# Optimization experiments

Hardware: AMD Instinct MI355X
Metric: run time of the kernel (lower is better)

The kernel has to match this reference:

```python
import jax, jax.numpy as jnp
import numpy as np

N, MA, F, NF = 512, 64, 128, 16
UPDATE_RATIO = 0.1
DECAY = 1.0
EPS = 1e-12  # avoids NaN grad of sqrt at self-distance 0 (torch diagonal is masked out by exp anyway)


def setup_inputs() -> dict:
    key = jax.random.key(0)
    ks = jax.random.split(key, 8)
    z = jax.random.randint(ks[0], (N, MA), 0, 10, dtype=jnp.int64) if jax.config.jax_enable_x64 else jax.random.randint(ks[0], (N, MA), 0, 10, dtype=jnp.int32)
    # pad last few atoms of each molecule with -1 to exercise the mask
    z = z.at[:, MA - 8:].set(-1)
    r = jax.random.normal(ks[1], (N, MA, 3), dtype=jnp.float32) * 3.0
    h = jax.random.normal(ks[2], (N, MA, F), dtype=jnp.float32)
    distances = jnp.linspace(0.5, 6.0, NF, dtype=jnp.float32)
    widths = jax.random.uniform(ks[3], (NF,), dtype=jnp.float32) * 0.5 + 0.5  # keep sigma > 0
    din = F * (1 + NF)  # 2176
    W1 = jax.random.normal(ks[4], (din, 512), dtype=jnp.float32) * (1.0 / np.sqrt(din))
    b1 = jnp.zeros((512,), dtype=jnp.float32)
    W2 = jax.random.normal(ks[5], (512, F), dtype=jnp.float32) * (1.0 / np.sqrt(512.0))
    b2 = jnp.zeros((F,), dtype=jnp.float32)
    return {"z": z, "r": r, "h": h, "distances": distances, "widths": widths,
            "W1": W1, "b1": b1, "W2": W2, "b2": b2}


def reference(z, r, h, distances, widths, W1, b1, W2, b2):
    n, ma = z.shape
    nf = distances.shape[0]
    # pairwise distance: (n, ma, ma)
    dv = r[:, :, None, :] - r[:, None, :, :]
    d = jnp.sqrt(jnp.sum(dv * dv, axis=-1) + EPS)
    mu = distances.reshape(1, nf, 1, 1)
    sigma = widths.reshape(1, nf, 1, 1)
    mask1 = (z > -1).astype(h.dtype)                      # (n, ma)
    pair_mask = mask1[:, :, None] * mask1[:, None, :]     # (n, ma, ma)
    # Gaussian RBF scores, masked: (n, nf, ma, ma)
    w = pair_mask[:, None] * jnp.exp(-((d[:, None] - mu) ** 2) / sigma) * 5.0
    # aggregate neighbor features: (n, ma, nf, F) -> (n, ma, nf*F)
    u = jnp.einsum('nfab,nbc->nafc', w, h).reshape(n, ma, nf * h.shape[-1])
    v = jnp.concatenate([h, u], axis=2)                   # (n, ma, F*(1+nf))
    v = jax.nn.silu(v @ W1 + b1) @ W2 + b2                # MLP 'net'
    h_new = h + v * UPDATE_RATIO * DECAY * mask1[:, :, None]
    return (z, r, h_new)
```

## Files before the change

### kernel.cpp

```cpp
#include <hip/hip_runtime.h>

#define MA 64
#define F 128
#define NF 16
#define HID 512
#define LDUB 144
#define LDWB 144
#define LDT1B 1040
#define UB0 0
#define UB1 9216
#define WL0 18432
#define WL1 27648

typedef float  float4v __attribute__((ext_vector_type(4)));
typedef short  short8  __attribute__((ext_vector_type(8)));
typedef int    int8v   __attribute__((ext_vector_type(8)));

static __device__ __forceinline__ unsigned int pack2bf(float x, float y) {
    unsigned int a = __float_as_uint(x) + 0x8000u;
    unsigned int b = __float_as_uint(y) + 0x8000u;
    return __builtin_amdgcn_perm(b, a, 0x07060302u);
}
static __device__ __forceinline__ unsigned short f2bf1(float x) {
    return (unsigned short)((__float_as_uint(x) + 0x8000u) >> 16);
}
static __device__ __forceinline__ unsigned int pk4fp8(float a, float b, float c, float d) {
    int p = __builtin_amdgcn_cvt_pk_fp8_f32(a, b, 0, false);
    p = __builtin_amdgcn_cvt_pk_fp8_f32(c, d, p, true);
    return (unsigned int)p;
}

#define LGKM_BAR() do {                                        \
    asm volatile("s_waitcnt lgkmcnt(0)" ::: "memory");         \
    __builtin_amdgcn_s_barrier();                              \
    asm volatile("" ::: "memory");                             \
} while (0)

__global__ void pack_frags(const float* __restrict__ W1, const float* __restrict__ W2,
                           unsigned char* __restrict__ w1p, unsigned short* __restrict__ w2p) {
    int gid  = blockIdx.x * 4 + (threadIdx.x >> 6);
    int lane = threadIdx.x & 63;
    int arow = lane & 15;
    int kq   = lane >> 4;
    if (gid < 544) {
        int kt = gid >> 5, jt = gid & 31;
        const float* base = W1 + (size_t)(kt * 128 + kq * 32) * HID + jt * 16 + arow;
        unsigned int o[8];
        #pragma unroll
        for (int p = 0; p < 8; p++)
            o[p] = pk4fp8(base[(p * 4 + 0) * HID], base[(p * 4 + 1) * HID],
                          base[(p * 4 + 2) * HID], base[(p * 4 + 3) * HID]);
        unsigned char* dst = w1p + ((size_t)gid * 64 + lane) * 32;
        *(uint4*)dst        = (uint4){o[0], o[1], o[2], o[3]};
        *(uint4*)(dst + 16) = (uint4){o[4], o[5], o[6], o[7]};
    } else if (gid < 544 + 128) {
        int g2 = gid - 544;
        int kt = g2 >> 3, mt = g2 & 7;
        const float* base = W2 + (size_t)(kt * 32 + kq * 8) * F + mt * 16 + arow;
        short8 o;
        #pragma unroll
        for (int j = 0; j < 8; j++) o[j] = (short)f2bf1(base[j * F]);
        *(short8*)(w2p + ((size_t)g2 * 64 + lane) * 8) = o;
    }
}

__launch_bounds__(1024, 4)
__global__ void node_conv_mfma(const int* __restrict__ z, const float* __restrict__ rr,
        const float* __restrict__ h, const float* __restrict__ dist,
        const float* __restrict__ wid, const float* __restrict__ b1,
        const float* __restrict__ b2,
        const unsigned char* __restrict__ w1p, const unsigned short* __restrict__ w2p,
        float* __restrict__ out) {
    const int n = blockIdx.x;
    const int tid = threadIdx.x;
    const int lane = tid & 63;
    const int wave = tid >> 6;
    const int arow = lane & 15;
    const int quad = lane >> 4;
    const int kgrp = quad * 8;
    const int whi = wave >> 1;
    const int wlo = wave & 1;

    __shared__ __attribute__((aligned(16))) unsigned char lds[66560];
    __shared__ float r_lds[MA][5];

    const int N = gridDim.x;
    const float* hg = h + (size_t)n * MA * F;

    if (tid < MA) {
        int zi = z[n * MA + tid];
        out[(size_t)n * MA + tid] = (float)zi;
        r_lds[tid][0] = rr[(n * MA + tid) * 3 + 0];
        r_lds[tid][1] = rr[(n * MA + tid) * 3 + 1];
        r_lds[tid][2] = rr[(n * MA + tid) * 3 + 2];
        r_lds[tid][3] = (zi > -1) ? 1.0f : 0.0f;
    }
    if (tid < MA * 3)
        out[(size_t)N * MA + (size_t)n * MA * 3 + tid] = rr[(size_t)n * MA * 3 + tid];

    for (int i = tid; i < MA * F / 4; i += 1024) {
        float4 v = ((const float4*)hg)[i];
        int a = i >> 5, c4 = (i & 31) * 4;
        *(unsigned int*)&lds[UB0 + a * LDUB + c4] = pk4fp8(v.x, v.y, v.z, v.w);
    }
    short8 ah[2];
    {
        int c = whi * 16 + arow;
        #pragma unroll
        for (int ks2 = 0; ks2 < 2; ks2++)
            #pragma unroll
            for (int j = 0; j < 8; j++)
                ah[ks2][j] = (short)f2bf1(hg[(size_t)(ks2 * 32 + kgrp + j) * F + c]);
    }
    __syncthreads();

    const int wa = tid >> 4;
    const int wb0 = (tid & 15) * 4;
    float dpre[4];
    {
        float ax = r_lds[wa][0], ay = r_lds[wa][1], az = r_lds[wa][2];
        float am = r_lds[wa][3];
        #pragma unroll
        for (int j = 0; j < 4; j++) {
            float dx = ax - r_lds[wb0 + j][0];
            float dy = ay - r_lds[wb0 + j][1];
            float dz = az - r_lds[wb0 + j][2];
            float d = sqrtf(dx * dx + dy * dy + dz * dz + 1e-12f);
            float mm = am * r_lds[wb0 + j][3];
            dpre[j] = d + (1.0f - mm) * 1e4f;
        }
    }

    {
        float mu = dist[0];
        float isg = 1.0f / wid[0];
        float e[4];
        #pragma unroll
        for (int j = 0; j < 4; j++) {
            float t = dpre[j] - mu;
            e[j] = 5.0f * __expf(-t * t * isg);
        }
        uint2 wp = { pack2bf(e[0], e[1]), pack2bf(e[2], e[3]) };
        *(uint2*)&lds[WL0 + wa * LDWB + wb0 * 2] = wp;
    }
    int8v afr[2];
    {
        const unsigned char* p0 = w1p + ((size_t)((wave * 2) * 64 + lane)) * 32;
        afr[0] = *(const int8v*)p0;
        afr[1] = *(const int8v*)(p0 + 2048);
    }
    LGKM_BAR();

    const float4v zf = {0.f, 0.f, 0.f, 0.f};
    float4v acc[2][4];
    #pragma unroll
    for (int i = 0; i < 2; i++)
        #pragma unroll
        for (int jv = 0; jv < 4; jv++) acc[i][jv] = zf;

    for (int f = 0; f <= NF; f++) {
        const int sel = f & 1;
        const int ubR = sel ? UB1 : UB0;
        const int ubW = sel ? UB0 : UB1;
        const int wlR = sel ? WL1 : WL0;
        const int wlW = sel ? WL0 : WL1;

        #pragma unroll
        for (int at = 0; at < 4; at++) {
            int8v bfr = *(const int8v*)&lds[ubR + (at * 16 + arow) * LDUB + quad * 32];
            acc[0][at] = __builtin_amdgcn_mfma_scale_f32_16x16x128_f8f6f4(
                afr[0], bfr, acc[0][at], 0, 0, 0, 127, 0, 127);
            acc[1][at] = __builtin_amdgcn_mfma_scale_f32_16x16x128_f8f6f4(
                afr[1], bfr, acc[1][at], 0, 0, 0, 127, 0, 127);
        }

        if (f < NF) {
            const unsigned char* pN = w1p + ((size_t)(((f + 1) * 32 + wave * 2) * 64 + lane)) * 32;
            afr[0] = *(const int8v*)pN;
            afr[1] = *(const int8v*)(pN + 2048);

            float4v ud0 = zf, ud1 = zf;
            #pragma unroll
            for (int ks2 = 0; ks2 < 2; ks2++) {
                short8 bw0 = *(const short8*)&lds[wlR + ((wlo * 2 + 0) * 16 + arow) * LDWB + (ks2 * 32 + kgrp) * 2];
                ud0 = __builtin_amdgcn_mfma_f32_16x16x32_bf16(ah[ks2], bw0, ud0, 0, 0, 0);
                short8 bw1 = *(const short8*)&lds[wlR + ((wlo * 2 + 1) * 16 + arow) * LDWB + (ks2 * 32 + kgrp) * 2];
                ud1 = __builtin_amdgcn_mfma_f32_16x16x32_bf16(ah[ks2], bw1, ud1, 0, 0, 0);
            }
            unsigned int u0 = pk4fp8(ud0[0], ud0[1], ud0[2], ud0[3]);
            unsigned int u1 = pk4fp8(ud1[0], ud1[1], ud1[2], ud1[3]);
            *(unsigned int*)&lds[ubW + ((wlo * 2 + 0) * 16 + arow) * LDUB + whi * 16 + quad * 4] = u0;
            *(unsigned int*)&lds[ubW + ((wlo * 2 + 1) * 16 + arow) * LDUB + whi * 16 + quad * 4] = u1;

            if (f <= NF - 2) {
                float mu = dist[f + 1];
                float isg = 1.0f / wid[f + 1];
                float e[4];
                #pragma unroll
                for (int j = 0; j < 4; j++) {
                    float t = dpre[j] - mu;
                    e[j] = 5.0f * __expf(-t * t * isg);
                }
                uint2 wp = { pack2bf(e[0], e[1]), pack2bf(e[2], e[3]) };
                *(uint2*)&lds[wlW + wa * LDWB + wb0 * 2] = wp;
            }
        }
        LGKM_BAR();
    }

    float4 b1v[2];
    #pragma unroll
    for (int mt = 0; mt < 2; mt++)
        b1v[mt] = *(const float4*)&b1[wave * 32 + mt * 16 + quad * 4];

    #pragma unroll
    for (int mt = 0; mt < 2; mt++) {
        #pragma unroll
        for (int at = 0; at < 4; at++) {
            float xs[4];
            #pragma unroll
            for (int r = 0; r < 4; r++) {
                float x = acc[mt][at][r] + ((const float*)&b1v[mt])[r];
                xs[r] = x / (1.0f + __expf(-x));
            }
            uint2 pv = { pack2bf(xs[0], xs[1]), pack2bf(xs[2], xs[3]) };
            *(uint2*)&lds[(at * 16 + arow) * LDT1B + (wave * 32 + mt * 16 + quad * 4) * 2] = pv;
        }
    }
    LGKM_BAR();

    float4v g2[2] = { zf, zf };

    short8 awA = *(const short8*)(w2p + ((size_t)(whi) * 64 + lane) * 8);
    #pragma unroll
    for (int ks2 = 0; ks2 < 8; ks2++) {
        const int k1 = 2 * ks2 + 1;
        short8 awB = *(const short8*)(w2p + ((size_t)(k1 * 8 + whi) * 64 + lane) * 8);
        #pragma unroll
        for (int j = 0; j < 2; j++) {
            short8 bt = *(const short8*)&lds[((wlo * 2 + j) * 16 + arow) * LDT1B + ((2 * ks2) * 32 + kgrp) * 2];
            g2[j] = __builtin_amdgcn_mfma_f32_16x16x32_bf16(awA, bt, g2[j], 0, 0, 0);
        }
        const int k2 = (ks2 < 7) ? 2 * ks2 + 2 : 0;
        awA = *(const short8*)(w2p + ((size_t)(k2 * 8 + whi) * 64 + lane) * 8);
        #pragma unroll
        for (int j = 0; j < 2; j++) {
            short8 bt = *(const short8*)&lds[((wlo * 2 + j) * 16 + arow) * LDT1B + ((2 * ks2 + 1) * 32 + kgrp) * 2];
            g2[j] = __builtin_amdgcn_mfma_f32_16x16x32_bf16(awB, bt, g2[j], 0, 0, 0);
        }
    }

    float* outh = out + (size_t)N * MA * 4 + (size_t)n * MA * F;
    const int c0 = whi * 16 + quad * 4;
    float4 b2v = *(const float4*)&b2[c0];
    #pragma unroll
    for (int j = 0; j < 2; j++) {
        int a = (wlo * 2 + j) * 16 + arow;
        float m = r_lds[a][3] * 0.1f;
        float4 hv = *(const float4*)&hg[a * F + c0];
        float4 res;
        res.x = hv.x + (g2[j][0] + b2v.x) * m;
        res.y = hv.y + (g2[j][1] + b2v.y) * m;
        res.z = hv.z + (g2[j][2] + b2v.z) * m;
        res.w = hv.w + (g2[j][3] + b2v.w) * m;
        *(float4*)&outh[(size_t)a * F + c0] = res;
    }
}

extern "C" void kernel_launch(void* const* d_in, const int* in_sizes, int n_in,
                              void* d_out, int out_size, void* d_ws, size_t ws_size,
                              hipStream_t stream) {
    const int*   z    = (const int*)d_in[0];
    const float* rr   = (const float*)d_in[1];
    const float* h    = (const float*)d_in[2];
    const float* dist = (const float*)d_in[3];
    const float* wid  = (const float*)d_in[4];
    const float* W1   = (const float*)d_in[5];
    const float* b1   = (const float*)d_in[6];
    const float* W2   = (const float*)d_in[7];
    const float* b2   = (const float*)d_in[8];
    float* out = (float*)d_out;

    int Nmol = in_sizes[0] / MA;

    unsigned char*  w1p = (unsigned char*)d_ws;
    unsigned short* w2p = (unsigned short*)(w1p + (size_t)544 * 64 * 32);

    pack_frags<<<168, 256, 0, stream>>>(W1, W2, w1p, w2p);
    node_conv_mfma<<<Nmol, 1024, 0, stream>>>(z, rr, h, dist, wid, b1, b2, w1p, w2p, out);
}
```

Before: 144.6 us.

## Split block into producer and consumer waves for RBF aggregation and W1 GEMM

Warp-specializes the 16-wave block. Waves 0-7 act as consumers that run the fp8 W1 MFMA accumulation with four 16-row hidden tiles each. Waves 8-15 act as producers that compute the RBF weights and the per-filter neighbour aggregation u into the double-buffered LDS tiles. Previously every wave did both jobs in each filter iteration; the split is meant to overlap the aggregation with the main GEMM. In exchange each consumer holds twice the accumulators and each producer holds four h fragments, which raises register pressure, and half of the waves now sit idle in each phase.

```diff
diff --git a/kernel.cpp b/kernel.cpp
--- a/kernel.cpp
+++ b/kernel.cpp
@@ -80,6 +80,7 @@
     const int kgrp = quad * 8;
     const int whi = wave >> 1;
     const int wlo = wave & 1;
+    const bool consumer = wave < 8;
 
     __shared__ __attribute__((aligned(16))) unsigned char lds[66560];
     __shared__ float r_lds[MA][5];
@@ -103,130 +104,158 @@
         int a = i >> 5, c4 = (i & 31) * 4;
         *(unsigned int*)&lds[UB0 + a * LDUB + c4] = pk4fp8(v.x, v.y, v.z, v.w);
     }
-    short8 ah[2];
-    {
-        int c = whi * 16 + arow;
-        #pragma unroll
-        for (int ks2 = 0; ks2 < 2; ks2++)
-            #pragma unroll
-            for (int j = 0; j < 8; j++)
-                ah[ks2][j] = (short)f2bf1(hg[(size_t)(ks2 * 32 + kgrp + j) * F + c]);
-    }
-    __syncthreads();
-
-    const int wa = tid >> 4;
-    const int wb0 = (tid & 15) * 4;
-    float dpre[4];
-    {
-        float ax = r_lds[wa][0], ay = r_lds[wa][1], az = r_lds[wa][2];
-        float am = r_lds[wa][3];
-        #pragma unroll
-        for (int j = 0; j < 4; j++) {
-            float dx = ax - r_lds[wb0 + j][0];
-            float dy = ay - r_lds[wb0 + j][1];
-            float dz = az - r_lds[wb0 + j][2];
-            float d = sqrtf(dx * dx + dy * dy + dz * dz + 1e-12f);
-            float mm = am * r_lds[wb0 + j][3];
-            dpre[j] = d + (1.0f - mm) * 1e4f;
-        }
-    }
-
-    {
-        float mu = dist[0];
-        float isg = 1.0f / wid[0];
-        float e[4];
-        #pragma unroll
-        for (int j = 0; j < 4; j++) {
-            float t = dpre[j] - mu;
-            e[j] = 5.0f * __expf(-t * t * isg);
-        }
-        uint2 wp = { pack2bf(e[0], e[1]), pack2bf(e[2], e[3]) };
-        *(uint2*)&lds[WL0 + wa * LDWB + wb0 * 2] = wp;
-    }
-    int8v afr[2];
-    {
-        const unsigned char* p0 = w1p + ((size_t)((wave * 2) * 64 + lane)) * 32;
-        afr[0] = *(const int8v*)p0;
-        afr[1] = *(const int8v*)(p0 + 2048);
-    }
-    LGKM_BAR();
 
     const float4v zf = {0.f, 0.f, 0.f, 0.f};
-    float4v acc[2][4];
-    #pragma unroll
-    for (int i = 0; i < 2; i++)
-        #pragma unroll
-        for (int jv = 0; jv < 4; jv++) acc[i][jv] = zf;
-
-    for (int f = 0; f <= NF; f++) {
-        const int sel = f & 1;
-        const int ubR = sel ? UB1 : UB0;
-        const int ubW = sel ? UB0 : UB1;
-        const int wlR = sel ? WL1 : WL0;
-        const int wlW = sel ? WL0 : WL1;
-
-        #pragma unroll
-        for (int at = 0; at < 4; at++) {
-            int8v bfr = *(const int8v*)&lds[ubR + (at * 16 + arow) * LDUB + quad * 32];
-            acc[0][at] = __builtin_amdgcn_mfma_scale_f32_16x16x128_f8f6f4(
-                afr[0], bfr, acc[0][at], 0, 0, 0, 127, 0, 127);
-            acc[1][at] = __builtin_amdgcn_mfma_scale_f32_16x16x128_f8f6f4(
-                afr[1], bfr, acc[1][at], 0, 0, 0, 127, 0, 127);
-        }
-
-        if (f < NF) {
-            const unsigned char* pN = w1p + ((size_t)(((f + 1) * 32 + wave * 2) * 64 + lane)) * 32;
-            afr[0] = *(const int8v*)pN;
-            afr[1] = *(const int8v*)(pN + 2048);
-
-            float4v ud0 = zf, ud1 = zf;
-            #pragma unroll
-            for (int ks2 = 0; ks2 < 2; ks2++) {
-                short8 bw0 = *(const short8*)&lds[wlR + ((wlo * 2 + 0) * 16 + arow) * LDWB + (ks2 * 32 + kgrp) * 2];
-                ud0 = __builtin_amdgcn_mfma_f32_16x16x32_bf16(ah[ks2], bw0, ud0, 0, 0, 0);
-                short8 bw1 = *(const short8*)&lds[wlR + ((wlo * 2 + 1) * 16 + arow) * LDWB + (ks2 * 32 + kgrp) * 2];
-                ud1 = __builtin_amdgcn_mfma_f32_16x16x32_bf16(ah[ks2], bw1, ud1, 0, 0, 0);
-            }
-            unsigned int u0 = pk4fp8(ud0[0], ud0[1], ud0[2], ud0[3]);
-            unsigned int u1 = pk4fp8(ud1[0], ud1[1], ud1[2], ud1[3]);
-            *(unsigned int*)&lds[ubW + ((wlo * 2 + 0) * 16 + arow) * LDUB + whi * 16 + quad * 4] = u0;
-            *(unsigned int*)&lds[ubW + ((wlo * 2 + 1) * 16 + arow) * LDUB + whi * 16 + quad * 4] = u1;
-
-            if (f <= NF - 2) {
-                float mu = dist[f + 1];
-                float isg = 1.0f / wid[f + 1];
-                float e[4];
+
+    if (consumer) {
+        const int ci = wave;
+        const int jbase = ci * 4;
+
+        int8v p0, p1, p2, p3;
+        {
+            const unsigned char* pp = w1p + ((size_t)(jbase * 64 + lane)) * 32;
+            p0 = *(const int8v*)pp;
+            p1 = *(const int8v*)(pp + 2048);
+        }
+        __syncthreads();
+        LGKM_BAR();
+
+        float4v acc[4][4];
+        #pragma unroll
+        for (int i = 0; i < 4; i++)
+            #pragma unroll
+            for (int jv = 0; jv < 4; jv++) acc[i][jv] = zf;
+
+        for (int f = 0; f <= NF; f++) {
+            const int ubR = (f & 1) ? UB1 : UB0;
+            const unsigned char* pseg = w1p + ((size_t)((f * 32 + jbase) * 64 + lane)) * 32;
+
+            p2 = *(const int8v*)(pseg + 2 * 2048);
+            p3 = *(const int8v*)(pseg + 3 * 2048);
+
+            #pragma unroll
+            for (int at = 0; at < 4; at++) {
+                int8v bfr = *(const int8v*)&lds[ubR + (at * 16 + arow) * LDUB + quad * 32];
+                acc[0][at] = __builtin_amdgcn_mfma_scale_f32_16x16x128_f8f6f4(
+                    p0, bfr, acc[0][at], 0, 0, 0, 127, 0, 127);
+                acc[1][at] = __builtin_amdgcn_mfma_scale_f32_16x16x128_f8f6f4(
+                    p1, bfr, acc[1][at], 0, 0, 0, 127, 0, 127);
+            }
+            #pragma unroll
+            for (int at = 0; at < 4; at++) {
+                int8v bfr = *(const int8v*)&lds[ubR + (at * 16 + arow) * LDUB + quad * 32];
+                acc[2][at] = __builtin_amdgcn_mfma_scale_f32_16x16x128_f8f6f4(
+                    p2, bfr, acc[2][at], 0, 0, 0, 127, 0, 127);
+                acc[3][at] = __builtin_amdgcn_mfma_scale_f32_16x16x128_f8f6f4(
+                    p3, bfr, acc[3][at], 0, 0, 0, 127, 0, 127);
+            }
+            if (f < NF) {
+                const unsigned char* pN = w1p + ((size_t)(((f + 1) * 32 + jbase) * 64 + lane)) * 32;
+                p0 = *(const int8v*)pN;
+                p1 = *(const int8v*)(pN + 2048);
+            }
+            LGKM_BAR();
+        }
+
+        #pragma unroll
+        for (int jj = 0; jj < 4; jj++) {
+            float4 b1v = *(const float4*)&b1[(jbase + jj) * 16 + quad * 4];
+            #pragma unroll
+            for (int at = 0; at < 4; at++) {
+                float xs[4];
                 #pragma unroll
-                for (int j = 0; j < 4; j++) {
-                    float t = dpre[j] - mu;
-                    e[j] = 5.0f * __expf(-t * t * isg);
+                for (int r = 0; r < 4; r++) {
+                    float x = acc[jj][at][r] + ((const float*)&b1v)[r];
+                    xs[r] = x / (1.0f + __expf(-x));
                 }
-                uint2 wp = { pack2bf(e[0], e[1]), pack2bf(e[2], e[3]) };
-                *(uint2*)&lds[wlW + wa * LDWB + wb0 * 2] = wp;
-            }
+                uint2 pv = { pack2bf(xs[0], xs[1]), pack2bf(xs[2], xs[3]) };
+                *(uint2*)&lds[(at * 16 + arow) * LDT1B + ((jbase + jj) * 16 + quad * 4) * 2] = pv;
+            }
+        }
+    } else {
+        const int pi = wave - 8;
+        const int uat = pi & 3;
+        const int uc0 = (pi >> 2) * 4;
+        const int pt  = tid - 512;
+        const int wa  = pt >> 3;
+        const int wb0 = (pt & 7) * 8;
+
+        short8 ah2[4][2];
+        #pragma unroll
+        for (int cc = 0; cc < 4; cc++) {
+            int c = (uc0 + cc) * 16 + arow;
+            #pragma unroll
+            for (int ks2 = 0; ks2 < 2; ks2++)
+                #pragma unroll
+                for (int j = 0; j < 8; j++)
+                    ah2[cc][ks2][j] = (short)f2bf1(hg[(size_t)(ks2 * 32 + kgrp + j) * F + c]);
+        }
+        __syncthreads();
+
+        float dpre[8];
+        {
+            float ax = r_lds[wa][0], ay = r_lds[wa][1], az = r_lds[wa][2];
+            float am = r_lds[wa][3];
+            #pragma unroll
+            for (int j = 0; j < 8; j++) {
+                float dx = ax - r_lds[wb0 + j][0];
+                float dy = ay - r_lds[wb0 + j][1];
+                float dz = az - r_lds[wb0 + j][2];
+                float d = sqrtf(dx * dx + dy * dy + dz * dz + 1e-12f);
+                float mm = am * r_lds[wb0 + j][3];
+                dpre[j] = d + (1.0f - mm) * 1e4f;
+            }
+        }
+        {
+            float mu = dist[0];
+            float isg = 1.0f / wid[0];
+            float e[8];
+            #pragma unroll
+            for (int j = 0; j < 8; j++) {
+                float t = dpre[j] - mu;
+                e[j] = 5.0f * __expf(-t * t * isg);
+            }
+            uint4 wp = { pack2bf(e[0], e[1]), pack2bf(e[2], e[3]),
+                         pack2bf(e[4], e[5]), pack2bf(e[6], e[7]) };
+            *(uint4*)&lds[WL0 + wa * LDWB + wb0 * 2] = wp;
         }
         LGKM_BAR();
-    }
-
-    float4 b1v[2];
-    #pragma unroll
-    for (int mt = 0; mt < 2; mt++)
-        b1v[mt] = *(const float4*)&b1[wave * 32 + mt * 16 + quad * 4];
-
-    #pragma unroll
-    for (int mt = 0; mt < 2; mt++) {
-        #pragma unroll
-        for (int at = 0; at < 4; at++) {
-            float xs[4];
-            #pragma unroll
-            for (int r = 0; r < 4; r++) {
-                float x = acc[mt][at][r] + ((const float*)&b1v[mt])[r];
-                xs[r] = x / (1.0f + __expf(-x));
-            }
-            uint2 pv = { pack2bf(xs[0], xs[1]), pack2bf(xs[2], xs[3]) };
-            *(uint2*)&lds[(at * 16 + arow) * LDT1B + (wave * 32 + mt * 16 + quad * 4) * 2] = pv;
-        }
-    }
+
+        for (int f = 0; f <= NF; f++) {
+            const int sel = f & 1;
+            const int ubW = sel ? UB0 : UB1;
+            const int wlR = sel ? WL1 : WL0;
+            const int wlW = sel ? WL0 : WL1;
+
+            if (f < NF) {
+                short8 bw0 = *(const short8*)&lds[wlR + (uat * 16 + arow) * LDWB + (0 * 32 + kgrp) * 2];
+                short8 bw1 = *(const short8*)&lds[wlR + (uat * 16 + arow) * LDWB + (1 * 32 + kgrp) * 2];
+                #pragma unroll
+                for (int cc = 0; cc < 4; cc++) {
+                    float4v ud = zf;
+                    ud = __builtin_amdgcn_mfma_f32_16x16x32_bf16(ah2[cc][0], bw0, ud, 0, 0, 0);
+                    ud = __builtin_amdgcn_mfma_f32_16x16x32_bf16(ah2[cc][1], bw1, ud, 0, 0, 0);
+                    unsigned int up = pk4fp8(ud[0], ud[1], ud[2], ud[3]);
+                    *(unsigned int*)&lds[ubW + (uat * 16 + arow) * LDUB + (uc0 + cc) * 16 + quad * 4] = up;
+                }
+                if (f <= NF - 2) {
+                    float mu = dist[f + 1];
+                    float isg = 1.0f / wid[f + 1];
+                    float e[8];
+                    #pragma unroll
+                    for (int j = 0; j < 8; j++) {
+                        float t = dpre[j] - mu;
+                        e[j] = 5.0f * __expf(-t * t * isg);
+                    }
+                    uint4 wp = { pack2bf(e[0], e[1]), pack2bf(e[2], e[3]),
+                                 pack2bf(e[4], e[5]), pack2bf(e[6], e[7]) };
+                    *(uint4*)&lds[wlW + wa * LDWB + wb0 * 2] = wp;
+                }
+            }
+            LGKM_BAR();
+        }
+    }
+
     LGKM_BAR();
 
     float4v g2[2] = { zf, zf };
```

Result: slower. 211.3 us (+46.1%).

## Process two feature chunks per pipeline stage to halve barrier count

Applied to the files above, without the earlier changes.

Restructures the per-filter loop so each iteration consumes two U chunks (two K-slices of the first-layer MFMA) and produces the next two, with doubled LDS buffers. This halves the number of workgroup barriers and adds more independent MFMA work between syncs, and the W1 fragment loads are split into two prefetched register sets. The cost is more LDS (73728 bytes), which may reduce occupancy, and more live registers, with a prologue and epilogue to handle the odd chunk count.

```diff
diff --git a/kernel.cpp b/kernel.cpp
--- a/kernel.cpp
+++ b/kernel.cpp
@@ -7,10 +7,12 @@
 #define LDUB 144
 #define LDWB 144
 #define LDT1B 1040
-#define UB0 0
-#define UB1 9216
-#define WL0 18432
-#define WL1 27648
+#define UBA 0
+#define UBB 18432
+#define WLA 36864
+#define WLB 55296
+#define UBT 9216
+#define WLT 9216
 
 typedef float  float4v __attribute__((ext_vector_type(4)));
 typedef short  short8  __attribute__((ext_vector_type(8)));
@@ -81,7 +83,7 @@
     const int whi = wave >> 1;
     const int wlo = wave & 1;
 
-    __shared__ __attribute__((aligned(16))) unsigned char lds[66560];
+    __shared__ __attribute__((aligned(16))) unsigned char lds[73728];
     __shared__ float r_lds[MA][5];
 
     const int N = gridDim.x;
@@ -101,7 +103,7 @@
     for (int i = tid; i < MA * F / 4; i += 1024) {
         float4 v = ((const float4*)hg)[i];
         int a = i >> 5, c4 = (i & 31) * 4;
-        *(unsigned int*)&lds[UB0 + a * LDUB + c4] = pk4fp8(v.x, v.y, v.z, v.w);
+        *(unsigned int*)&lds[UBA + a * LDUB + c4] = pk4fp8(v.x, v.y, v.z, v.w);
     }
     short8 ah[2];
     {
@@ -111,6 +113,12 @@
             #pragma unroll
             for (int j = 0; j < 8; j++)
                 ah[ks2][j] = (short)f2bf1(hg[(size_t)(ks2 * 32 + kgrp + j) * F + c]);
+    }
+    int8v p0, p1, q0, q1;
+    {
+        const unsigned char* pp = w1p + ((size_t)((wave * 2) * 64 + lane)) * 32;
+        p0 = *(const int8v*)pp;
+        p1 = *(const int8v*)(pp + 2048);
     }
     __syncthreads();
 
@@ -131,9 +139,9 @@
         }
     }
 
-    {
-        float mu = dist[0];
-        float isg = 1.0f / wid[0];
+    auto EXPW = [&](int fidx, int wlOff) {
+        float mu = dist[fidx];
+        float isg = 1.0f / wid[fidx];
         float e[4];
         #pragma unroll
         for (int j = 0; j < 4; j++) {
@@ -141,72 +149,88 @@
             e[j] = 5.0f * __expf(-t * t * isg);
         }
         uint2 wp = { pack2bf(e[0], e[1]), pack2bf(e[2], e[3]) };
-        *(uint2*)&lds[WL0 + wa * LDWB + wb0 * 2] = wp;
-    }
-    int8v afr[2];
-    {
-        const unsigned char* p0 = w1p + ((size_t)((wave * 2) * 64 + lane)) * 32;
-        afr[0] = *(const int8v*)p0;
-        afr[1] = *(const int8v*)(p0 + 2048);
-    }
+        *(uint2*)&lds[wlOff + wa * LDWB + wb0 * 2] = wp;
+    };
+    const float4v zf = {0.f, 0.f, 0.f, 0.f};
+    auto UG = [&](int wlOff, int ubOff) {
+        float4v ud0 = zf, ud1 = zf;
+        #pragma unroll
+        for (int ks2 = 0; ks2 < 2; ks2++) {
+            short8 bw0 = *(const short8*)&lds[wlOff + ((wlo * 2 + 0) * 16 + arow) * LDWB + (ks2 * 32 + kgrp) * 2];
+            ud0 = __builtin_amdgcn_mfma_f32_16x16x32_bf16(ah[ks2], bw0, ud0, 0, 0, 0);
+            short8 bw1 = *(const short8*)&lds[wlOff + ((wlo * 2 + 1) * 16 + arow) * LDWB + (ks2 * 32 + kgrp) * 2];
+            ud1 = __builtin_amdgcn_mfma_f32_16x16x32_bf16(ah[ks2], bw1, ud1, 0, 0, 0);
+        }
+        unsigned int u0 = pk4fp8(ud0[0], ud0[1], ud0[2], ud0[3]);
+        unsigned int u1 = pk4fp8(ud1[0], ud1[1], ud1[2], ud1[3]);
+        *(unsigned int*)&lds[ubOff + ((wlo * 2 + 0) * 16 + arow) * LDUB + whi * 16 + quad * 4] = u0;
+        *(unsigned int*)&lds[ubOff + ((wlo * 2 + 1) * 16 + arow) * LDUB + whi * 16 + quad * 4] = u1;
+    };
+
+    EXPW(0, WLB);
+    EXPW(1, WLA);
+    EXPW(2, WLA + WLT);
     LGKM_BAR();
-
-    const float4v zf = {0.f, 0.f, 0.f, 0.f};
+    UG(WLB, UBA + UBT);
+    LGKM_BAR();
+
     float4v acc[2][4];
     #pragma unroll
     for (int i = 0; i < 2; i++)
         #pragma unroll
         for (int jv = 0; jv < 4; jv++) acc[i][jv] = zf;
 
-    for (int f = 0; f <= NF; f++) {
-        const int sel = f & 1;
-        const int ubR = sel ? UB1 : UB0;
-        const int ubW = sel ? UB0 : UB1;
-        const int wlR = sel ? WL1 : WL0;
-        const int wlW = sel ? WL0 : WL1;
-
+    for (int i = 0; i < 8; i++) {
+        const int sel = i & 1;
+        const int ubR = sel ? UBB : UBA;
+        const int ubW = sel ? UBA : UBB;
+        const int wlR = sel ? WLB : WLA;
+        const int wlW = sel ? WLA : WLB;
+
+        {
+            const unsigned char* pq = w1p + ((size_t)(((2 * i + 1) * 32 + wave * 2) * 64 + lane)) * 32;
+            q0 = *(const int8v*)pq;
+            q1 = *(const int8v*)(pq + 2048);
+        }
         #pragma unroll
         for (int at = 0; at < 4; at++) {
             int8v bfr = *(const int8v*)&lds[ubR + (at * 16 + arow) * LDUB + quad * 32];
             acc[0][at] = __builtin_amdgcn_mfma_scale_f32_16x16x128_f8f6f4(
-                afr[0], bfr, acc[0][at], 0, 0, 0, 127, 0, 127);
+                p0, bfr, acc[0][at], 0, 0, 0, 127, 0, 127);
             acc[1][at] = __builtin_amdgcn_mfma_scale_f32_16x16x128_f8f6f4(
-                afr[1], bfr, acc[1][at], 0, 0, 0, 127, 0, 127);
-        }
-
-        if (f < NF) {
-            const unsigned char* pN = w1p + ((size_t)(((f + 1) * 32 + wave * 2) * 64 + lane)) * 32;
-            afr[0] = *(const int8v*)pN;
-            afr[1] = *(const int8v*)(pN + 2048);
-
-            float4v ud0 = zf, ud1 = zf;
-            #pragma unroll
-            for (int ks2 = 0; ks2 < 2; ks2++) {
-                short8 bw0 = *(const short8*)&lds[wlR + ((wlo * 2 + 0) * 16 + arow) * LDWB + (ks2 * 32 + kgrp) * 2];
-                ud0 = __builtin_amdgcn_mfma_f32_16x16x32_bf16(ah[ks2], bw0, ud0, 0, 0, 0);
-                short8 bw1 = *(const short8*)&lds[wlR + ((wlo * 2 + 1) * 16 + arow) * LDWB + (ks2 * 32 + kgrp) * 2];
-                ud1 = __builtin_amdgcn_mfma_f32_16x16x32_bf16(ah[ks2], bw1, ud1, 0, 0, 0);
-            }
-            unsigned int u0 = pk4fp8(ud0[0], ud0[1], ud0[2], ud0[3]);
-            unsigned int u1 = pk4fp8(ud1[0], ud1[1], ud1[2], ud1[3]);
-            *(unsigned int*)&lds[ubW + ((wlo * 2 + 0) * 16 + arow) * LDUB + whi * 16 + quad * 4] = u0;
-            *(unsigned int*)&lds[ubW + ((wlo * 2 + 1) * 16 + arow) * LDUB + whi * 16 + quad * 4] = u1;
-
-            if (f <= NF - 2) {
-                float mu = dist[f + 1];
-                float isg = 1.0f / wid[f + 1];
-                float e[4];
-                #pragma unroll
-                for (int j = 0; j < 4; j++) {
-                    float t = dpre[j] - mu;
-                    e[j] = 5.0f * __expf(-t * t * isg);
-                }
-                uint2 wp = { pack2bf(e[0], e[1]), pack2bf(e[2], e[3]) };
-                *(uint2*)&lds[wlW + wa * LDWB + wb0 * 2] = wp;
-            }
-        }
+                p1, bfr, acc[1][at], 0, 0, 0, 127, 0, 127);
+        }
+        #pragma unroll
+        for (int at = 0; at < 4; at++) {
+            int8v bfr = *(const int8v*)&lds[ubR + UBT + (at * 16 + arow) * LDUB + quad * 32];
+            acc[0][at] = __builtin_amdgcn_mfma_scale_f32_16x16x128_f8f6f4(
+                q0, bfr, acc[0][at], 0, 0, 0, 127, 0, 127);
+            acc[1][at] = __builtin_amdgcn_mfma_scale_f32_16x16x128_f8f6f4(
+                q1, bfr, acc[1][at], 0, 0, 0, 127, 0, 127);
+        }
+        {
+            const unsigned char* pp = w1p + ((size_t)(((2 * i + 2) * 32 + wave * 2) * 64 + lane)) * 32;
+            p0 = *(const int8v*)pp;
+            p1 = *(const int8v*)(pp + 2048);
+        }
+
+        UG(wlR, ubW);
+        if (2 * i + 2 <= NF - 1) UG(wlR + WLT, ubW + UBT);
+        if (2 * i + 3 <= NF - 1) EXPW(2 * i + 3, wlW);
+        if (2 * i + 4 <= NF - 1) EXPW(2 * i + 4, wlW + WLT);
+
         LGKM_BAR();
     }
+
+    #pragma unroll
+    for (int at = 0; at < 4; at++) {
+        int8v bfr = *(const int8v*)&lds[UBA + (at * 16 + arow) * LDUB + quad * 32];
+        acc[0][at] = __builtin_amdgcn_mfma_scale_f32_16x16x128_f8f6f4(
+            p0, bfr, acc[0][at], 0, 0, 0, 127, 0, 127);
+        acc[1][at] = __builtin_amdgcn_mfma_scale_f32_16x16x128_f8f6f4(
+            p1, bfr, acc[1][at], 0, 0, 0, 127, 0, 127);
+    }
+    LGKM_BAR();
 
     float4 b1v[2];
     #pragma unroll
```

Result: no change. 146.5 us (+1.4%).
